# Optimization experiments

Measured on AMD Instinct MI355X. Metric: run time of the kernel, lower is better.

The kernel has to match this reference:

```python
import jax, jax.numpy as jnp
import numpy as np

N, S, K, C_IN, C_OUT = 100000, 50000, 32, 128, 128


def setup_inputs() -> dict:
    key = jax.random.key(0)
    k1, k2, k3, k4, k5 = jax.random.split(key, 5)
    word_vec = jax.random.normal(k1, (N, C_IN), dtype=jnp.float32)
    # unique source indices (torch scatter-set with duplicate idx is nondeterministic)
    src_idx = jax.random.permutation(k2, N)[:S].astype(jnp.int64)
    neighs_idx = jax.random.randint(k3, (S, K), 0, N).astype(jnp.int64)
    src_mask = jax.random.randint(k4, (S, K), 0, 2).astype(jnp.int32)
    # xavier-uniform-style Linear weight, zero bias
    limit = float(np.sqrt(6.0 / (C_IN + C_OUT)))
    W_before = jax.random.uniform(k5, (C_OUT, C_IN), minval=-limit, maxval=limit, dtype=jnp.float32)
    b_before = jnp.zeros((C_OUT,), dtype=jnp.float32)
    return {"word_vec": word_vec, "src_idx": src_idx, "neighs_idx": neighs_idx,
            "src_mask": src_mask, "W_before": W_before, "b_before": b_before}


def reference(word_vec, src_idx, neighs_idx, src_mask, W_before, b_before):
    # dropout in eval mode -> identity
    supports = word_vec                                   # [N, C_in]
    q = supports[src_idx]                                 # [S, C_in]
    k = supports[neighs_idx]                              # [S, K, C_in]
    scores = jnp.einsum('sc,skc->sk', q, k) * 5.0         # [S, K]
    scores = jnp.where(src_mask == 1, scores, jnp.float32(-1e6))
    probs = jax.nn.softmax(scores, axis=-1)               # [S, K]
    # proj_before: Linear + LeakyReLU(0.2)
    supports = jax.nn.leaky_relu(word_vec @ W_before.T + b_before, negative_slope=0.2)  # [N, C_out]
    agg = jnp.einsum('sk,skc->sc', probs, supports[neighs_idx])  # [S, C_out]
    supports = supports.at[src_idx].set(agg)
    return supports
```

## Files before the change

kernel.cpp:

```cpp
#include <hip/hip_runtime.h>

#define NN 100000
#define SS 50000
#define KK 32
#define CC 128
#define RPB 160
#define LDA 136

typedef _Float16 f16x8 __attribute__((ext_vector_type(8)));
typedef _Float16 f16x4 __attribute__((ext_vector_type(4)));
typedef _Float16 f16x2 __attribute__((ext_vector_type(2)));
typedef float f32x4 __attribute__((ext_vector_type(4)));


__global__ __launch_bounds__(256) void proj_kernel(
    const float* __restrict__ wv,
    const float* __restrict__ W,
    const float* __restrict__ bias,
    _Float16* __restrict__ T,
    float* __restrict__ out)
{
    __shared__ _Float16 sA[RPB][LDA];

    const int t = threadIdx.x;
    const int base = blockIdx.x * RPB;

    #pragma unroll 4
    for (int i = 0; i < 20; i++) {
        const int idx = i * 256 + t;
        const int row = idx >> 5;
        const int c4 = (idx & 31) * 4;
        const float4 v = *(const float4*)(wv + (size_t)(base + row) * CC + c4);
        f16x4 h;
        h[0] = (_Float16)v.x; h[1] = (_Float16)v.y;
        h[2] = (_Float16)v.z; h[3] = (_Float16)v.w;
        *(f16x4*)&sA[row][c4] = h;
        *(f16x4*)(T + (size_t)(base + row) * 256 + c4) = h;
    }

    const int w = t >> 6;
    const int l = t & 63;
    const int q = l >> 4;
    const int c = l & 15;

    f16x8 bf[2][4];
    float bo[2];
    #pragma unroll
    for (int nch = 0; nch < 2; nch++) {
        const int n = w * 32 + nch * 16 + c;
        bo[nch] = bias[n];
        const float* Wr = W + (size_t)n * CC;
        #pragma unroll
        for (int kc = 0; kc < 4; kc++) {
            const int k0 = kc * 32 + q * 8;
            const float4 w0 = *(const float4*)(Wr + k0);
            const float4 w1 = *(const float4*)(Wr + k0 + 4);
            f16x8 b;
            b[0] = (_Float16)w0.x; b[1] = (_Float16)w0.y;
            b[2] = (_Float16)w0.z; b[3] = (_Float16)w0.w;
            b[4] = (_Float16)w1.x; b[5] = (_Float16)w1.y;
            b[6] = (_Float16)w1.z; b[7] = (_Float16)w1.w;
            bf[nch][kc] = b;
        }
    }
    __syncthreads();

    #pragma unroll 2
    for (int sub = 0; sub < RPB / 16; sub++) {
        const int rl = sub * 16 + c;

        f16x8 af[4];
        #pragma unroll
        for (int kc = 0; kc < 4; kc++)
            af[kc] = *(const f16x8*)&sA[rl][kc * 32 + q * 8];

        f32x4 acc[2] = {{0.f, 0.f, 0.f, 0.f}, {0.f, 0.f, 0.f, 0.f}};
        #pragma unroll
        for (int kc = 0; kc < 4; kc++) {
            acc[0] = __builtin_amdgcn_mfma_f32_16x16x32_f16(af[kc], bf[0][kc], acc[0], 0, 0, 0);
            acc[1] = __builtin_amdgcn_mfma_f32_16x16x32_f16(af[kc], bf[1][kc], acc[1], 0, 0, 0);
        }

        #pragma unroll
        for (int nch = 0; nch < 2; nch++) {
            const int col = w * 32 + nch * 16 + c;
            #pragma unroll
            for (int r = 0; r < 4; r++) {
                const int row = base + sub * 16 + q * 4 + r;
                float v = acc[nch][r] + bo[nch];
                v = v > 0.f ? v : 0.2f * v;
                out[(size_t)row * CC + col] = v;
                T[(size_t)row * 256 + 128 + col] = (_Float16)v;
            }
        }
    }
}

__global__ __launch_bounds__(256) void attn_kernel(
    const _Float16* __restrict__ T,
    const int* __restrict__ src_idx,
    const int* __restrict__ neighs,
    const int* __restrict__ mask,
    float* __restrict__ out)
{
    const int s = (blockIdx.x * 256 + threadIdx.x) >> 6;
    if (s >= SS) return;
    const int lane = threadIdx.x & 63;
    const int c = lane & 15;
    const int r = lane >> 4;

    int nbv[8], mv[8];
    #pragma unroll
    for (int ch = 0; ch < 8; ch++) {
        nbv[ch] = neighs[s * KK + ch * 4 + r];
        mv[ch]  = mask[s * KK + ch * 4 + r];
    }
    const int src = src_idx[s];
    const f16x8 qh = *(const f16x8*)(T + (size_t)src * 256 + c * 8);

    f16x8 kh[8];
    #pragma unroll
    for (int ch = 0; ch < 8; ch++) {
        const int row = (mv[ch] == 1) ? nbv[ch] : src;
        kh[ch] = *(const f16x8*)(T + (size_t)row * 256 + c * 8);
    }

    float sc[8];
    #pragma unroll
    for (int ch = 0; ch < 8; ch++) {
        float d = 0.f;
        #pragma unroll
        for (int j = 0; j < 4; j++) {
            f16x2 qa; qa[0] = qh[2 * j];     qa[1] = qh[2 * j + 1];
            f16x2 ka; ka[0] = kh[ch][2 * j]; ka[1] = kh[ch][2 * j + 1];
            d = __builtin_amdgcn_fdot2(qa, ka, d, false);
        }
        d += __shfl_xor(d, 1);
        d += __shfl_xor(d, 2);
        d += __shfl_xor(d, 4);
        d += __shfl_xor(d, 8);
        sc[ch] = (mv[ch] == 1) ? d * 5.0f : -1e6f;
    }

    float mx = sc[0];
    #pragma unroll
    for (int ch = 1; ch < 8; ch++) mx = fmaxf(mx, sc[ch]);
    mx = fmaxf(mx, __shfl_xor(mx, 16));
    mx = fmaxf(mx, __shfl_xor(mx, 32));

    float p[8];
    float sum = 0.f;
    #pragma unroll
    for (int ch = 0; ch < 8; ch++) {
        p[ch] = __expf(sc[ch] - mx);
        sum += p[ch];
    }
    sum += __shfl_xor(sum, 16);
    sum += __shfl_xor(sum, 32);
    const float inv = 1.0f / sum;
    #pragma unroll
    for (int ch = 0; ch < 8; ch++) p[ch] *= inv;

    f16x8 vv[8];
    #pragma unroll
    for (int ch = 0; ch < 8; ch++) {
        const int row = (p[ch] != 0.f) ? nbv[ch] : src;
        vv[ch] = *(const f16x8*)(T + (size_t)row * 256 + 128 + c * 8);
    }

    float acc[8] = {0.f, 0.f, 0.f, 0.f, 0.f, 0.f, 0.f, 0.f};
    #pragma unroll
    for (int ch = 0; ch < 8; ch++) {
        #pragma unroll
        for (int j = 0; j < 8; j++)
            acc[j] += p[ch] * (float)vv[ch][j];
    }

    #pragma unroll
    for (int j = 0; j < 8; j++) {
        acc[j] += __shfl_xor(acc[j], 16);
        acc[j] += __shfl_xor(acc[j], 32);
    }

    *((float2*)(out + (size_t)src * CC) + c * 4 + r) =
        make_float2(acc[r * 2], acc[r * 2 + 1]);
}

extern "C" void kernel_launch(void* const* d_in, const int* in_sizes, int n_in,
                              void* d_out, int out_size, void* d_ws, size_t ws_size,
                              hipStream_t stream)
{
    const float* wv   = (const float*)d_in[0];
    const int*   src  = (const int*)d_in[1];
    const int*   nei  = (const int*)d_in[2];
    const int*   msk  = (const int*)d_in[3];
    const float* W    = (const float*)d_in[4];
    const float* bias = (const float*)d_in[5];
    float* out = (float*)d_out;
    _Float16* T = (_Float16*)d_ws;

    proj_kernel<<<NN / RPB, 256, 0, stream>>>(wv, W, bias, T, out);
    attn_kernel<<<(SS * 64) / 256, 256, 0, stream>>>(T, src, nei, msk, out);
}
```

Before: 180.7 us.

## Issue key and value gathers together; stage projection output through LDS

The attention kernel now computes each neighbour's row offset once and issues the key and value gathers back to back, before the softmax. Previously the value loads waited until the probabilities were known, so the two memory round trips ran in sequence. Masked neighbours now load the source row, or the real neighbour when every mask bit is zero, and 32-bit offsets and a fast reciprocal are used. The projection kernel writes its fp16 output into shared memory and copies it to global memory with coalesced vector stores, which adds barriers and higher register pressure under launch bounds of 4.

```diff
diff --git a/kernel.cpp b/kernel.cpp
--- a/kernel.cpp
+++ b/kernel.cpp
@@ -74,6 +74,8 @@
         for (int kc = 0; kc < 4; kc++)
             af[kc] = *(const f16x8*)&sA[rl][kc * 32 + q * 8];
 
+        __syncthreads();
+
         f32x4 acc[2] = {{0.f, 0.f, 0.f, 0.f}, {0.f, 0.f, 0.f, 0.f}};
         #pragma unroll
         for (int kc = 0; kc < 4; kc++) {
@@ -85,18 +87,27 @@
         for (int nch = 0; nch < 2; nch++) {
             const int col = w * 32 + nch * 16 + c;
             #pragma unroll
-            for (int r = 0; r < 4; r++) {
-                const int row = base + sub * 16 + q * 4 + r;
-                float v = acc[nch][r] + bo[nch];
+            for (int rr = 0; rr < 4; rr++) {
+                const int rowl = sub * 16 + q * 4 + rr;
+                float v = acc[nch][rr] + bo[nch];
                 v = v > 0.f ? v : 0.2f * v;
-                out[(size_t)row * CC + col] = v;
-                T[(size_t)row * 256 + 128 + col] = (_Float16)v;
+                out[(size_t)(base + rowl) * CC + col] = v;
+                sA[rowl][col] = (_Float16)v;
             }
         }
     }
+
+    __syncthreads();
+    #pragma unroll 4
+    for (int i = 0; i < 20; i++) {
+        const int idx = i * 256 + t;
+        const int row = idx >> 5;
+        const int c4 = (idx & 31) * 4;
+        *(f16x4*)(T + (size_t)(base + row) * 256 + 128 + c4) = *(const f16x4*)&sA[row][c4];
+    }
 }
 
-__global__ __launch_bounds__(256) void attn_kernel(
+__global__ __launch_bounds__(256, 4) void attn_kernel(
     const _Float16* __restrict__ T,
     const int* __restrict__ src_idx,
     const int* __restrict__ neighs,
@@ -109,21 +120,37 @@
     const int c = lane & 15;
     const int r = lane >> 4;
 
-    int nbv[8], mv[8];
+    int nbv[8];
+    int mbits = 0;
     #pragma unroll
     for (int ch = 0; ch < 8; ch++) {
         nbv[ch] = neighs[s * KK + ch * 4 + r];
-        mv[ch]  = mask[s * KK + ch * 4 + r];
+        mbits |= (mask[s * KK + ch * 4 + r] & 1) << ch;
     }
     const int src = src_idx[s];
-    const f16x8 qh = *(const f16x8*)(T + (size_t)src * 256 + c * 8);
-
+
+    const bool havem = (__any(mbits) != 0);
+
+    const char* Tb = (const char*)T;
+    const unsigned cb = (unsigned)c << 4;
+
+    unsigned off[8];
+    #pragma unroll
+    for (int ch = 0; ch < 8; ch++) {
+        const int row = (((mbits >> ch) & 1) || !havem) ? nbv[ch] : src;
+        off[ch] = ((unsigned)row << 9) + cb;
+    }
+
+    const f16x8 qh = *(const f16x8*)(Tb + (((unsigned)src << 9) + cb));
     f16x8 kh[8];
     #pragma unroll
-    for (int ch = 0; ch < 8; ch++) {
-        const int row = (mv[ch] == 1) ? nbv[ch] : src;
-        kh[ch] = *(const f16x8*)(T + (size_t)row * 256 + c * 8);
-    }
+    for (int ch = 0; ch < 8; ch++)
+        kh[ch] = *(const f16x8*)(Tb + off[ch]);
+    f16x8 vv[8];
+    #pragma unroll
+    for (int ch = 0; ch < 8; ch++)
+        vv[ch] = *(const f16x8*)(Tb + off[ch] + 256);
+    __builtin_amdgcn_sched_barrier(0);
 
     float sc[8];
     #pragma unroll
@@ -139,7 +166,7 @@
         d += __shfl_xor(d, 2);
         d += __shfl_xor(d, 4);
         d += __shfl_xor(d, 8);
-        sc[ch] = (mv[ch] == 1) ? d * 5.0f : -1e6f;
+        sc[ch] = ((mbits >> ch) & 1) ? d * 5.0f : -1e6f;
     }
 
     float mx = sc[0];
@@ -157,16 +184,9 @@
     }
     sum += __shfl_xor(sum, 16);
     sum += __shfl_xor(sum, 32);
-    const float inv = 1.0f / sum;
+    const float inv = __builtin_amdgcn_rcpf(sum);
     #pragma unroll
     for (int ch = 0; ch < 8; ch++) p[ch] *= inv;
-
-    f16x8 vv[8];
-    #pragma unroll
-    for (int ch = 0; ch < 8; ch++) {
-        const int row = (p[ch] != 0.f) ? nbv[ch] : src;
-        vv[ch] = *(const f16x8*)(T + (size_t)row * 256 + 128 + c * 8);
-    }
 
     float acc[8] = {0.f, 0.f, 0.f, 0.f, 0.f, 0.f, 0.f, 0.f};
     #pragma unroll
```

Measured after the change: 190.0 us. 1.05x slower.
